# Performance work log

Measured on AMD Instinct MI355X. Metric: run time of the kernel, lower is better.

The kernel has to match this reference:

```python
import jax, jax.numpy as jnp
import numpy as np

B, TQ, TK = 4, 128, 512
DQ = DK = DV = H = 1024


def setup_inputs() -> dict:
    key = jax.random.key(0)
    ks = jax.random.split(key, 7)
    s = 0.05  # keep tanh out of saturation
    return {
        "query": jax.random.normal(ks[0], (B, TQ, DQ), dtype=jnp.float32),
        "key": jax.random.normal(ks[1], (B, TK, DK), dtype=jnp.float32),
        "value": jax.random.normal(ks[2], (B, TK, DV), dtype=jnp.float32),
        "Wq": jax.random.normal(ks[3], (DQ, H), dtype=jnp.float32) * s,
        "bq": jax.random.normal(ks[4], (H,), dtype=jnp.float32) * s,
        "Wk": jax.random.normal(ks[5], (DK, H), dtype=jnp.float32) * s,
        "v": jax.random.normal(ks[6], (H,), dtype=jnp.float32) * s,
    }


def reference(query, key, value, Wq, bq, Wk, v):
    # additive (Bahdanau) attention
    wq = jnp.einsum("bqd,dh->bqh", query, Wq) + bq      # [B,Tq,H]
    uh = jnp.einsum("bkd,dh->bkh", key, Wk)             # [B,Tk,H]
    # broadcast add -> [B,Tq,Tk,H], tanh, project to scalar score
    scores = jnp.einsum("bqkh,h->bqk",
                        jnp.tanh(wq[:, :, None, :] + uh[:, None, :, :]), v)
    attn = jax.nn.softmax(scores, axis=-1)              # [B,Tq,Tk]
    h = jnp.einsum("bqk,bkv->bqv", attn, value)         # [B,Tq,Dv]
    return h, attn
```

## Files before the change

kernel.cpp:

```cpp
#include <hip/hip_runtime.h>
#include <hip/hip_bf16.h>

typedef float f32x4 __attribute__((ext_vector_type(4)));
typedef float f32x2 __attribute__((ext_vector_type(2)));
typedef short s16x8 __attribute__((ext_vector_type(8)));
typedef short s16x4 __attribute__((ext_vector_type(4)));

#define NB  4
#define NTQ 128
#define NTK 512
#define NH  1024

__device__ __forceinline__ unsigned short f2bf(float x) {
    unsigned u = __builtin_bit_cast(unsigned, x);
    u += 0x7FFFu + ((u >> 16) & 1u);
    return (unsigned short)(u >> 16);
}

#define K2E  2.8853900817779268f

#define GLD16(gp, lp) __builtin_amdgcn_global_load_lds( \
    (const __attribute__((address_space(1))) unsigned int*)(gp), \
    (__attribute__((address_space(3))) unsigned int*)(lp), 16, 0, 0)

__global__ __launch_bounds__(256) void prep_kernel(
    const float* __restrict__ Q, const float* __restrict__ K,
    const float* __restrict__ Wq, const float* __restrict__ Wk,
    const float* __restrict__ value,
    short* __restrict__ Qb, short* __restrict__ Kb,
    short* __restrict__ WqT, short* __restrict__ WkT, short* __restrict__ valT)
{
    const int t = threadIdx.x, bx = blockIdx.x;
    if (bx < 640) {
        const float* src; short* dst; size_t base;
        if (bx < 128) { src = Q; dst = Qb; base = (size_t)bx * 4096; }
        else          { src = K; dst = Kb; base = (size_t)(bx - 128) * 4096; }
        #pragma unroll
        for (int i = 0; i < 4; ++i) {
            const size_t off = base + (size_t)(i * 256 + t) * 4;
            const float4 vv = *(const float4*)(src + off);
            s16x4 o = { (short)f2bf(vv.x), (short)f2bf(vv.y),
                        (short)f2bf(vv.z), (short)f2bf(vv.w) };
            *(s16x4*)(dst + off) = o;
        }
        return;
    }
    __shared__ float tile[64][65];
    const int i = bx - 640;
    const float* src; short* dst; int Cs, Rs, r0, c0;
    if (i < 256)      { src = Wq; dst = WqT; Cs = 1024; Rs = 1024; r0 = (i >> 4) * 64; c0 = (i & 15) * 64; }
    else if (i < 512) { const int j = i - 256; src = Wk; dst = WkT; Cs = 1024; Rs = 1024; r0 = (j >> 4) * 64; c0 = (j & 15) * 64; }
    else {
        const int j = i - 512, b = j >> 7, ti = j & 127;
        src = value + (size_t)b * 512 * 1024; dst = valT + (size_t)b * 1024 * 512;
        Cs = 1024; Rs = 512; r0 = (ti >> 4) * 64; c0 = (ti & 15) * 64;
    }
    {
        const int c = (t & 15) * 4;
        #pragma unroll
        for (int it = 0; it < 4; ++it) {
            const int r = (t >> 4) + it * 16;
            const float4 vv = *(const float4*)(src + (size_t)(r0 + r) * Cs + c0 + c);
            tile[r][c + 0] = vv.x; tile[r][c + 1] = vv.y;
            tile[r][c + 2] = vv.z; tile[r][c + 3] = vv.w;
        }
    }
    __syncthreads();
    {
        const int r = (t & 15) * 4;
        #pragma unroll
        for (int it = 0; it < 4; ++it) {
            const int c = (t >> 4) + it * 16;
            s16x4 o = { (short)f2bf(tile[r + 0][c]), (short)f2bf(tile[r + 1][c]),
                        (short)f2bf(tile[r + 2][c]), (short)f2bf(tile[r + 3][c]) };
            *(s16x4*)(dst + (size_t)(c0 + c) * Rs + r0 + r) = o;
        }
    }
}

__global__ __launch_bounds__(256) void mm_kernel(
    const short* __restrict__ Qb, const short* __restrict__ Kb,
    const short* __restrict__ WqT, const short* __restrict__ WkT,
    const float* __restrict__ bq,
    float* __restrict__ Ea_out, float* __restrict__ EbT)
{
    __shared__ short ldsA[2][128][64];
    __shared__ short ldsB[2][64][64];
    const int t = threadIdx.x;
    const int bx0 = blockIdx.x;
    const int bx = (bx0 & 7) * 40 + (bx0 >> 3);
    const bool g1 = bx < 64;
    const short *A, *B; int m0, n0;
    if (g1) { A = Qb; B = WqT; m0 = (bx >> 4) * 128; n0 = (bx & 15) * 64; }
    else    { const int i = bx - 64; A = Kb; B = WkT; m0 = (i >> 4) * 128; n0 = (i & 15) * 64; }
    A += (size_t)m0 * 1024; B += (size_t)n0 * 1024;

    f32x4 acc[4][2];
    #pragma unroll
    for (int i = 0; i < 4; ++i)
        #pragma unroll
        for (int j = 0; j < 2; ++j) acc[i][j] = f32x4{0.f, 0.f, 0.f, 0.f};

    const int lane = t & 63, wid = t >> 6;
    const int wr = wid >> 1, wc = wid & 1;
    const int fr = lane & 15, fko = (lane >> 4) * 16;

    #define STAGE_MM(buf, k0) do {                                              \
        _Pragma("unroll")                                                       \
        for (int it = 0; it < 4; ++it) {                                        \
            const int idx = it * 256 + t;                                       \
            const int row = idx >> 3, c16 = idx & 7;                            \
            const int sc = c16 ^ (row & 7);                                     \
            GLD16(A + (size_t)row * 1024 + (k0) + sc * 8,                       \
                  &ldsA[buf][0][0] + idx * 8);                                  \
        }                                                                       \
        _Pragma("unroll")                                                       \
        for (int it = 0; it < 2; ++it) {                                        \
            const int idx = it * 256 + t;                                       \
            const int row = idx >> 3, c16 = idx & 7;                            \
            const int sc = c16 ^ (row & 7);                                     \
            GLD16(B + (size_t)row * 1024 + (k0) + sc * 8,                       \
                  &ldsB[buf][0][0] + idx * 8);                                  \
        }                                                                       \
    } while (0)

    #define COMPUTE_MM(buf) do {                                                \
        _Pragma("unroll")                                                       \
        for (int kk = 0; kk < 2; ++kk) {                                        \
            s16x8 af[4], bfv[2];                                                \
            _Pragma("unroll")                                                   \
            for (int i = 0; i < 4; ++i) {                                       \
                const int rowA = wr * 64 + i * 16 + fr;                         \
                int offA = rowA * 128 + kk * 64 + fko; offA ^= (rowA & 7) << 4; \
                af[i] = *(const s16x8*)((const char*)&ldsA[buf][0][0] + offA);  \
            }                                                                   \
            _Pragma("unroll")                                                   \
            for (int ni = 0; ni < 2; ++ni) {                                    \
                const int rowB = wc * 32 + ni * 16 + fr;                        \
                int offB = rowB * 128 + kk * 64 + fko; offB ^= (rowB & 7) << 4; \
                bfv[ni] = *(const s16x8*)((const char*)&ldsB[buf][0][0] + offB);\
            }                                                                   \
            _Pragma("unroll")                                                   \
            for (int mi = 0; mi < 4; ++mi)                                      \
                _Pragma("unroll")                                               \
                for (int ni = 0; ni < 2; ++ni)                                  \
                    acc[mi][ni] = __builtin_amdgcn_mfma_f32_16x16x32_bf16(      \
                                      af[mi], bfv[ni], acc[mi][ni], 0, 0, 0);   \
        }                                                                       \
    } while (0)

    STAGE_MM(0, 0);
    __syncthreads();
    int cur = 0;
    for (int s = 0; s < 15; ++s) {
        STAGE_MM(cur ^ 1, (s + 1) * 64);
        COMPUTE_MM(cur);
        __syncthreads();
        cur ^= 1;
    }
    COMPUTE_MM(cur);

    const int row0 = (lane >> 4) * 4;
    if (g1) {
        #pragma unroll
        for (int ni = 0; ni < 2; ++ni) {
            const int n = n0 + wc * 32 + ni * 16 + fr;
            const float bias = bq[n];
            #pragma unroll
            for (int mi = 0; mi < 4; ++mi) {
                const int m = m0 + wr * 64 + mi * 16 + row0;
                #pragma unroll
                for (int j = 0; j < 4; ++j)
                    Ea_out[(size_t)(m + j) * 1024 + n] =
                        __builtin_amdgcn_exp2f(K2E * (acc[mi][ni][j] + bias));
            }
        }
    } else {
        #pragma unroll
        for (int mi = 0; mi < 4; ++mi) {
            const int m = m0 + wr * 64 + mi * 16 + row0;
            const int b = m >> 9, kk = m & 511;
            #pragma unroll
            for (int ni = 0; ni < 2; ++ni) {
                const int n = n0 + wc * 32 + ni * 16 + fr;
                f32x4 ev;
                #pragma unroll
                for (int j = 0; j < 4; ++j)
                    ev[j] = __builtin_amdgcn_exp2f(K2E * acc[mi][ni][j]);
                *(f32x4*)&EbT[((size_t)b * 1024 + n) * 512 + kk] = ev;
            }
        }
    }
    #undef STAGE_MM
    #undef COMPUTE_MM
}

__global__ __launch_bounds__(512) void scores_partial(
    const float* __restrict__ EbT, const float* __restrict__ Ea,
    const float* __restrict__ v, float* __restrict__ partial)
{
    __shared__ float4 s_ea4[64][2];
    __shared__ float  s_v[64];
    const int t = threadIdx.x, bx = blockIdx.x;
    const int hc = bx & 15, bq8 = bx >> 4;
    const int b = bq8 >> 4, q8 = bq8 & 15;
    const int bq0 = b * 128 + q8 * 8, h0 = hc * 64;

    if (t < 64) {
        const int h = h0 + t;
        s_ea4[t][0] = make_float4(Ea[(size_t)(bq0 + 0) * 1024 + h],
                                  Ea[(size_t)(bq0 + 1) * 1024 + h],
                                  Ea[(size_t)(bq0 + 2) * 1024 + h],
                                  Ea[(size_t)(bq0 + 3) * 1024 + h]);
        s_ea4[t][1] = make_float4(Ea[(size_t)(bq0 + 4) * 1024 + h],
                                  Ea[(size_t)(bq0 + 5) * 1024 + h],
                                  Ea[(size_t)(bq0 + 6) * 1024 + h],
                                  Ea[(size_t)(bq0 + 7) * 1024 + h]);
        s_v[t] = v[h];
    }
    __syncthreads();

    const float* up = EbT + ((size_t)b * 1024 + h0) * 512 + t;
    f32x2 a0 = {0.f, 0.f}, a1 = {0.f, 0.f}, a2 = {0.f, 0.f}, a3 = {0.f, 0.f};
    #pragma unroll 4
    for (int hh = 0; hh < 64; ++hh) {
        const float  eb = up[(size_t)hh * 512];
        const float4 e0 = s_ea4[hh][0];
        const float4 e1 = s_ea4[hh][1];
        const float  vv = s_v[hh];
        f32x2 p0 = f32x2{e0.x, e0.y} * eb + 1.0f;
        f32x2 p1 = f32x2{e0.z, e0.w} * eb + 1.0f;
        f32x2 p2 = f32x2{e1.x, e1.y} * eb + 1.0f;
        f32x2 p3 = f32x2{e1.z, e1.w} * eb + 1.0f;
        f32x2 r0 = {__builtin_amdgcn_rcpf(p0.x), __builtin_amdgcn_rcpf(p0.y)};
        f32x2 r1 = {__builtin_amdgcn_rcpf(p1.x), __builtin_amdgcn_rcpf(p1.y)};
        f32x2 r2 = {__builtin_amdgcn_rcpf(p2.x), __builtin_amdgcn_rcpf(p2.y)};
        f32x2 r3 = {__builtin_amdgcn_rcpf(p3.x), __builtin_amdgcn_rcpf(p3.y)};
        a0 += r0 * vv;
        a1 += r1 * vv;
        a2 += r2 * vv;
        a3 += r3 * vv;
    }
    partial[((size_t)(bq0 + 0) * 16 + hc) * 512 + t] = a0.x;
    partial[((size_t)(bq0 + 1) * 16 + hc) * 512 + t] = a0.y;
    partial[((size_t)(bq0 + 2) * 16 + hc) * 512 + t] = a1.x;
    partial[((size_t)(bq0 + 3) * 16 + hc) * 512 + t] = a1.y;
    partial[((size_t)(bq0 + 4) * 16 + hc) * 512 + t] = a2.x;
    partial[((size_t)(bq0 + 5) * 16 + hc) * 512 + t] = a2.y;
    partial[((size_t)(bq0 + 6) * 16 + hc) * 512 + t] = a3.x;
    partial[((size_t)(bq0 + 7) * 16 + hc) * 512 + t] = a3.y;
}

__global__ __launch_bounds__(512) void softmax_kernel(
    const float* __restrict__ partial, float* __restrict__ attn_out,
    short* __restrict__ attnb)
{
    __shared__ float s_red[16];
    const int t = threadIdx.x, bqi = blockIdx.x;
    const float* p = partial + (size_t)bqi * 16 * 512;
    float zs = 0.f;
    #pragma unroll
    for (int j = 0; j < 16; ++j) zs += p[j * 512 + t];
    const float z = -2.0f * zs;

    const int lane = t & 63, wid = t >> 6;
    float m = z;
    #pragma unroll
    for (int off = 32; off > 0; off >>= 1)
        m = fmaxf(m, __shfl_xor(m, off, 64));
    if (lane == 0) s_red[wid] = m;
    __syncthreads();
    if (t < 64) {
        float mm = (t < 8) ? s_red[t] : -3.0e38f;
        #pragma unroll
        for (int off = 4; off > 0; off >>= 1)
            mm = fmaxf(mm, __shfl_xor(mm, off, 64));
        if (t == 0) s_red[8] = mm;
    }
    __syncthreads();
    const float pr = __expf(z - s_red[8]);
    float s = pr;
    #pragma unroll
    for (int off = 32; off > 0; off >>= 1)
        s += __shfl_xor(s, off, 64);
    if (lane == 0) s_red[wid] = s;
    __syncthreads();
    if (t < 64) {
        float ss = (t < 8) ? s_red[t] : 0.f;
        #pragma unroll
        for (int off = 4; off > 0; off >>= 1)
            ss += __shfl_xor(ss, off, 64);
        if (t == 0) s_red[9] = ss;
    }
    __syncthreads();
    const float attn = pr * (1.0f / s_red[9]);
    attn_out[(size_t)bqi * 512 + t] = attn;
    attnb[(size_t)bqi * 512 + t] = (short)f2bf(attn);
}

__global__ __launch_bounds__(256) void pv_gemm(
    const short* __restrict__ attnb, const short* __restrict__ valT,
    float* __restrict__ outh)
{
    __shared__ short ldsA[2][128][64];
    __shared__ short ldsB[2][64][64];
    const int t = threadIdx.x, bx = blockIdx.x;
    const int b = bx >> 4, nt = bx & 15;
    const int n0 = nt * 64;
    const short* A = attnb + (size_t)b * 128 * 512;
    const short* B = valT + (size_t)b * 1024 * 512 + (size_t)n0 * 512;

    f32x4 acc[4][2];
    #pragma unroll
    for (int i = 0; i < 4; ++i)
        #pragma unroll
        for (int j = 0; j < 2; ++j) acc[i][j] = f32x4{0.f, 0.f, 0.f, 0.f};

    const int lane = t & 63, wid = t >> 6;
    const int wr = wid >> 1, wc = wid & 1;
    const int fr = lane & 15, fko = (lane >> 4) * 16;

    #define STAGE_PV(buf, k0) do {                                              \
        _Pragma("unroll")                                                       \
        for (int it = 0; it < 4; ++it) {                                        \
            const int idx = it * 256 + t;                                       \
            const int row = idx >> 3, c16 = idx & 7;                            \
            const int sc = c16 ^ (row & 7);                                     \
            GLD16(A + (size_t)row * 512 + (k0) + sc * 8,                        \
                  &ldsA[buf][0][0] + idx * 8);                                  \
        }                                                                       \
        _Pragma("unroll")                                                       \
        for (int it = 0; it < 2; ++it) {                                        \
            const int idx = it * 256 + t;                                       \
            const int row = idx >> 3, c16 = idx & 7;                            \
            const int sc = c16 ^ (row & 7);                                     \
            GLD16(B + (size_t)row * 512 + (k0) + sc * 8,                        \
                  &ldsB[buf][0][0] + idx * 8);                                  \
        }                                                                       \
    } while (0)

    #define COMPUTE_PV(buf) do {                                                \
        _Pragma("unroll")                                                       \
        for (int kk = 0; kk < 2; ++kk) {                                        \
            s16x8 af[4], bfv[2];                                                \
            _Pragma("unroll")                                                   \
            for (int i = 0; i < 4; ++i) {                                       \
                const int rowA = wr * 64 + i * 16 + fr;                         \
                int offA = rowA * 128 + kk * 64 + fko; offA ^= (rowA & 7) << 4; \
                af[i] = *(const s16x8*)((const char*)&ldsA[buf][0][0] + offA);  \
            }                                                                   \
            _Pragma("unroll")                                                   \
            for (int ni = 0; ni < 2; ++ni) {                                    \
                const int rowB = wc * 32 + ni * 16 + fr;                        \
                int offB = rowB * 128 + kk * 64 + fko; offB ^= (rowB & 7) << 4; \
                bfv[ni] = *(const s16x8*)((const char*)&ldsB[buf][0][0] + offB);\
            }                                                                   \
            _Pragma("unroll")                                                   \
            for (int mi = 0; mi < 4; ++mi)                                      \
                _Pragma("unroll")                                               \
                for (int ni = 0; ni < 2; ++ni)                                  \
                    acc[mi][ni] = __builtin_amdgcn_mfma_f32_16x16x32_bf16(      \
                                      af[mi], bfv[ni], acc[mi][ni], 0, 0, 0);   \
        }                                                                       \
    } while (0)

    STAGE_PV(0, 0);
    __syncthreads();
    int cur = 0;
    for (int s = 0; s < 7; ++s) {
        STAGE_PV(cur ^ 1, (s + 1) * 64);
        COMPUTE_PV(cur);
        __syncthreads();
        cur ^= 1;
    }
    COMPUTE_PV(cur);

    const int row0 = (lane >> 4) * 4;
    #pragma unroll
    for (int ni = 0; ni < 2; ++ni) {
        const int n = n0 + wc * 32 + ni * 16 + fr;
        #pragma unroll
        for (int mi = 0; mi < 4; ++mi) {
            const int m = wr * 64 + mi * 16 + row0;
            #pragma unroll
            for (int j = 0; j < 4; ++j)
                outh[(size_t)(b * 128 + m + j) * 1024 + n] = acc[mi][ni][j];
        }
    }
    #undef STAGE_PV
    #undef COMPUTE_PV
}

extern "C" void kernel_launch(void* const* d_in, const int* in_sizes, int n_in,
                              void* d_out, int out_size, void* d_ws, size_t ws_size,
                              hipStream_t stream)
{
    const float* query = (const float*)d_in[0];
    const float* key   = (const float*)d_in[1];
    const float* value = (const float*)d_in[2];
    const float* Wq    = (const float*)d_in[3];
    const float* bq    = (const float*)d_in[4];
    const float* Wk    = (const float*)d_in[5];
    const float* v     = (const float*)d_in[6];
    float* out = (float*)d_out;

    char* w = (char*)d_ws;
    float* ws_Ea  = (float*)w;
    float* ws_EbT = (float*)(w + (2u << 20));
    short* Qb     = (short*)(w + (10u << 20));
    short* Kb     = (short*)(w + (11u << 20));
    short* WqT    = (short*)(w + (15u << 20));
    short* WkT    = (short*)(w + (17u << 20));
    short* valT   = (short*)(w + (19u << 20));
    short* attnb  = (short*)(w + (23u << 20));
    float* part   = (float*)(w + (24u << 20));

    float* out_h    = out;
    float* out_attn = out + (size_t)NB * NTQ * NH;

    prep_kernel   <<<dim3(1664), dim3(256), 0, stream>>>(query, key, Wq, Wk, value,
                                                         Qb, Kb, WqT, WkT, valT);
    mm_kernel     <<<dim3(320),  dim3(256), 0, stream>>>(Qb, Kb, WqT, WkT, bq, ws_Ea, ws_EbT);
    scores_partial<<<dim3(1024), dim3(512), 0, stream>>>(ws_EbT, ws_Ea, v, part);
    softmax_kernel<<<dim3(512),  dim3(512), 0, stream>>>(part, out_attn, attnb);
    pv_gemm       <<<dim3(64),   dim3(256), 0, stream>>>(attnb, valT, out_h);
}
```

Measured before the change: 72.07 us.

## Fuse scores and softmax into one kernel, store exp(2*uh) as bf16

Merges the partial-score and softmax kernels into a single kernel. Each block now handles two query rows across the full hidden dimension, so the partial buffer and its extra launch go away. The exp(2*uh) intermediate is stored as bf16 rather than fp32, halving its write and read traffic. In exchange each block does 1024 serial iterations with only 256 blocks, reusing each EbT load for just 2 queries instead of 8, and bf16 rounding adds error to the scores.

Measured after the change: 87.49 us. 21.4% more time.

```diff
diff --git a/kernel.cpp b/kernel.cpp
--- a/kernel.cpp
+++ b/kernel.cpp
@@ -82,7 +82,7 @@
     const short* __restrict__ Qb, const short* __restrict__ Kb,
     const short* __restrict__ WqT, const short* __restrict__ WkT,
     const float* __restrict__ bq,
-    float* __restrict__ Ea_out, float* __restrict__ EbT)
+    float* __restrict__ Ea_out, unsigned short* __restrict__ EbT)
 {
     __shared__ short ldsA[2][128][64];
     __shared__ short ldsB[2][64][64];
@@ -183,11 +183,11 @@
             #pragma unroll
             for (int ni = 0; ni < 2; ++ni) {
                 const int n = n0 + wc * 32 + ni * 16 + fr;
-                f32x4 ev;
+                s16x4 ev;
                 #pragma unroll
                 for (int j = 0; j < 4; ++j)
-                    ev[j] = __builtin_amdgcn_exp2f(K2E * acc[mi][ni][j]);
-                *(f32x4*)&EbT[((size_t)b * 1024 + n) * 512 + kk] = ev;
+                    ev[j] = (short)f2bf(__builtin_amdgcn_exp2f(K2E * acc[mi][ni][j]));
+                *(s16x4*)&EbT[((size_t)b * 1024 + n) * 512 + kk] = ev;
             }
         }
     }
@@ -195,107 +195,73 @@
     #undef COMPUTE_MM
 }
 
-__global__ __launch_bounds__(512) void scores_partial(
-    const float* __restrict__ EbT, const float* __restrict__ Ea,
-    const float* __restrict__ v, float* __restrict__ partial)
-{
-    __shared__ float4 s_ea4[64][2];
-    __shared__ float  s_v[64];
+__global__ __launch_bounds__(512) void scores_softmax(
+    const unsigned short* __restrict__ EbT, const float* __restrict__ Ea,
+    const float* __restrict__ v,
+    float* __restrict__ attn_out, short* __restrict__ attnb)
+{
+    __shared__ float4 s_eav[1024];
+    __shared__ float2 s_red[8];
     const int t = threadIdx.x, bx = blockIdx.x;
-    const int hc = bx & 15, bq8 = bx >> 4;
-    const int b = bq8 >> 4, q8 = bq8 & 15;
-    const int bq0 = b * 128 + q8 * 8, h0 = hc * 64;
-
-    if (t < 64) {
-        const int h = h0 + t;
-        s_ea4[t][0] = make_float4(Ea[(size_t)(bq0 + 0) * 1024 + h],
-                                  Ea[(size_t)(bq0 + 1) * 1024 + h],
-                                  Ea[(size_t)(bq0 + 2) * 1024 + h],
-                                  Ea[(size_t)(bq0 + 3) * 1024 + h]);
-        s_ea4[t][1] = make_float4(Ea[(size_t)(bq0 + 4) * 1024 + h],
-                                  Ea[(size_t)(bq0 + 5) * 1024 + h],
-                                  Ea[(size_t)(bq0 + 6) * 1024 + h],
-                                  Ea[(size_t)(bq0 + 7) * 1024 + h]);
-        s_v[t] = v[h];
-    }
-    __syncthreads();
-
-    const float* up = EbT + ((size_t)b * 1024 + h0) * 512 + t;
-    f32x2 a0 = {0.f, 0.f}, a1 = {0.f, 0.f}, a2 = {0.f, 0.f}, a3 = {0.f, 0.f};
-    #pragma unroll 4
-    for (int hh = 0; hh < 64; ++hh) {
-        const float  eb = up[(size_t)hh * 512];
-        const float4 e0 = s_ea4[hh][0];
-        const float4 e1 = s_ea4[hh][1];
-        const float  vv = s_v[hh];
-        f32x2 p0 = f32x2{e0.x, e0.y} * eb + 1.0f;
-        f32x2 p1 = f32x2{e0.z, e0.w} * eb + 1.0f;
-        f32x2 p2 = f32x2{e1.x, e1.y} * eb + 1.0f;
-        f32x2 p3 = f32x2{e1.z, e1.w} * eb + 1.0f;
-        f32x2 r0 = {__builtin_amdgcn_rcpf(p0.x), __builtin_amdgcn_rcpf(p0.y)};
-        f32x2 r1 = {__builtin_amdgcn_rcpf(p1.x), __builtin_amdgcn_rcpf(p1.y)};
-        f32x2 r2 = {__builtin_amdgcn_rcpf(p2.x), __builtin_amdgcn_rcpf(p2.y)};
-        f32x2 r3 = {__builtin_amdgcn_rcpf(p3.x), __builtin_amdgcn_rcpf(p3.y)};
-        a0 += r0 * vv;
-        a1 += r1 * vv;
-        a2 += r2 * vv;
-        a3 += r3 * vv;
-    }
-    partial[((size_t)(bq0 + 0) * 16 + hc) * 512 + t] = a0.x;
-    partial[((size_t)(bq0 + 1) * 16 + hc) * 512 + t] = a0.y;
-    partial[((size_t)(bq0 + 2) * 16 + hc) * 512 + t] = a1.x;
-    partial[((size_t)(bq0 + 3) * 16 + hc) * 512 + t] = a1.y;
-    partial[((size_t)(bq0 + 4) * 16 + hc) * 512 + t] = a2.x;
-    partial[((size_t)(bq0 + 5) * 16 + hc) * 512 + t] = a2.y;
-    partial[((size_t)(bq0 + 6) * 16 + hc) * 512 + t] = a3.x;
-    partial[((size_t)(bq0 + 7) * 16 + hc) * 512 + t] = a3.y;
-}
-
-__global__ __launch_bounds__(512) void softmax_kernel(
-    const float* __restrict__ partial, float* __restrict__ attn_out,
-    short* __restrict__ attnb)
-{
-    __shared__ float s_red[16];
-    const int t = threadIdx.x, bqi = blockIdx.x;
-    const float* p = partial + (size_t)bqi * 16 * 512;
-    float zs = 0.f;
-    #pragma unroll
-    for (int j = 0; j < 16; ++j) zs += p[j * 512 + t];
-    const float z = -2.0f * zs;
-
+    const int b = bx >> 6, q2 = bx & 63;
+    const int bq0 = b * 128 + q2 * 2;
     const int lane = t & 63, wid = t >> 6;
-    float m = z;
-    #pragma unroll
-    for (int off = 32; off > 0; off >>= 1)
-        m = fmaxf(m, __shfl_xor(m, off, 64));
-    if (lane == 0) s_red[wid] = m;
-    __syncthreads();
-    if (t < 64) {
-        float mm = (t < 8) ? s_red[t] : -3.0e38f;
-        #pragma unroll
-        for (int off = 4; off > 0; off >>= 1)
-            mm = fmaxf(mm, __shfl_xor(mm, off, 64));
-        if (t == 0) s_red[8] = mm;
-    }
-    __syncthreads();
-    const float pr = __expf(z - s_red[8]);
-    float s = pr;
-    #pragma unroll
-    for (int off = 32; off > 0; off >>= 1)
-        s += __shfl_xor(s, off, 64);
-    if (lane == 0) s_red[wid] = s;
-    __syncthreads();
-    if (t < 64) {
-        float ss = (t < 8) ? s_red[t] : 0.f;
-        #pragma unroll
-        for (int off = 4; off > 0; off >>= 1)
-            ss += __shfl_xor(ss, off, 64);
-        if (t == 0) s_red[9] = ss;
-    }
-    __syncthreads();
-    const float attn = pr * (1.0f / s_red[9]);
-    attn_out[(size_t)bqi * 512 + t] = attn;
-    attnb[(size_t)bqi * 512 + t] = (short)f2bf(attn);
+
+    for (int h = t; h < 1024; h += 512)
+        s_eav[h] = make_float4(Ea[(size_t)(bq0 + 0) * 1024 + h],
+                               Ea[(size_t)(bq0 + 1) * 1024 + h],
+                               v[h], 0.f);
+    __syncthreads();
+
+    const unsigned short* up = EbT + (size_t)b * 1024 * 512 + t;
+    f32x2 acc = {0.f, 0.f};
+    #pragma unroll 8
+    for (int h = 0; h < 1024; ++h) {
+        const unsigned ebb = up[(size_t)h * 512];
+        const float eb = __builtin_bit_cast(float, ebb << 16);
+        const float4 e = s_eav[h];
+        f32x2 p = f32x2{e.x, e.y} * eb + 1.0f;
+        f32x2 r = {__builtin_amdgcn_rcpf(p.x), __builtin_amdgcn_rcpf(p.y)};
+        acc += r * e.z;
+    }
+    const f32x2 z = acc * -2.0f;
+
+    f32x2 m = z;
+    #pragma unroll
+    for (int off = 32; off > 0; off >>= 1) {
+        m.x = fmaxf(m.x, __shfl_xor(m.x, off, 64));
+        m.y = fmaxf(m.y, __shfl_xor(m.y, off, 64));
+    }
+    if (lane == 0) s_red[wid] = make_float2(m.x, m.y);
+    __syncthreads();
+    float mx0 = s_red[0].x, mx1 = s_red[0].y;
+    #pragma unroll
+    for (int w = 1; w < 8; ++w) {
+        mx0 = fmaxf(mx0, s_red[w].x);
+        mx1 = fmaxf(mx1, s_red[w].y);
+    }
+    const float p0 = __expf(z.x - mx0);
+    const float p1 = __expf(z.y - mx1);
+    __syncthreads();
+
+    float s0l = p0, s1l = p1;
+    #pragma unroll
+    for (int off = 32; off > 0; off >>= 1) {
+        s0l += __shfl_xor(s0l, off, 64);
+        s1l += __shfl_xor(s1l, off, 64);
+    }
+    if (lane == 0) s_red[wid] = make_float2(s0l, s1l);
+    __syncthreads();
+    float s0 = 0.f, s1 = 0.f;
+    #pragma unroll
+    for (int w = 0; w < 8; ++w) { s0 += s_red[w].x; s1 += s_red[w].y; }
+
+    const float a0 = p0 * (1.0f / s0);
+    const float a1 = p1 * (1.0f / s1);
+    attn_out[(size_t)(bq0 + 0) * 512 + t] = a0;
+    attn_out[(size_t)(bq0 + 1) * 512 + t] = a1;
+    attnb[(size_t)(bq0 + 0) * 512 + t] = (short)f2bf(a0);
+    attnb[(size_t)(bq0 + 1) * 512 + t] = (short)f2bf(a1);
 }
 
 __global__ __launch_bounds__(256) void pv_gemm(
@@ -405,15 +371,14 @@
     float* out = (float*)d_out;
 
     char* w = (char*)d_ws;
-    float* ws_Ea  = (float*)w;
-    float* ws_EbT = (float*)(w + (2u << 20));
-    short* Qb     = (short*)(w + (10u << 20));
-    short* Kb     = (short*)(w + (11u << 20));
-    short* WqT    = (short*)(w + (15u << 20));
-    short* WkT    = (short*)(w + (17u << 20));
-    short* valT   = (short*)(w + (19u << 20));
-    short* attnb  = (short*)(w + (23u << 20));
-    float* part   = (float*)(w + (24u << 20));
+    float*          ws_Ea  = (float*)w;
+    unsigned short* ws_EbT = (unsigned short*)(w + (2u << 20));
+    short* Qb     = (short*)(w + (6u << 20));
+    short* Kb     = (short*)(w + (7u << 20));
+    short* WqT    = (short*)(w + (11u << 20));
+    short* WkT    = (short*)(w + (13u << 20));
+    short* valT   = (short*)(w + (15u << 20));
+    short* attnb  = (short*)(w + (19u << 20));
 
     float* out_h    = out;
     float* out_attn = out + (size_t)NB * NTQ * NH;
@@ -421,7 +386,6 @@
     prep_kernel   <<<dim3(1664), dim3(256), 0, stream>>>(query, key, Wq, Wk, value,
                                                          Qb, Kb, WqT, WkT, valT);
     mm_kernel     <<<dim3(320),  dim3(256), 0, stream>>>(Qb, Kb, WqT, WkT, bq, ws_Ea, ws_EbT);
-    scores_partial<<<dim3(1024), dim3(512), 0, stream>>>(ws_EbT, ws_Ea, v, part);
-    softmax_kernel<<<dim3(512),  dim3(512), 0, stream>>>(part, out_attn, attnb);
+    scores_softmax<<<dim3(256),  dim3(512), 0, stream>>>(ws_EbT, ws_Ea, v, out_attn, attnb);
     pv_gemm       <<<dim3(64),   dim3(256), 0, stream>>>(attnb, valT, out_h);
 }
```
